# Performance work log

Hardware: AMD Instinct MI355X
Metric: run time of the kernel (lower is better)

The kernel has to match this reference:

```python
import jax, jax.numpy as jnp
import numpy as np

B, I, O = 262144, 128, 128


def setup_inputs() -> dict:
    key = jax.random.key(0)
    k1, k2, k3, k4 = jax.random.split(key, 4)
    # coordinate-like inputs in [-1, 1]
    x = jax.random.uniform(k1, (B, I), dtype=jnp.float32, minval=-1.0, maxval=1.0)
    # complex weight w = s * exp(i*theta): |w| = s (close to 1 so |w|^x stays stable),
    # angle(w) = theta, matching the torch init where complex_weight = cos(a) + i sin(a).
    theta = jax.random.uniform(k2, (O, I), dtype=jnp.float32, minval=-np.pi, maxval=np.pi)
    scale = jnp.exp(0.1 * jax.random.normal(k3, (O, I), dtype=jnp.float32))
    w_real = scale * jnp.cos(theta)
    w_imag = scale * jnp.sin(theta)
    bias = jax.random.uniform(k4, (O,), dtype=jnp.float32, minval=-np.pi, maxval=np.pi)
    return {"x": x, "w_real": w_real, "w_imag": w_imag, "bias": bias}


def reference(x, w_real, w_imag, bias):
    # complex_weight.abs() and .angle() from real/imag components
    abs_w = jnp.sqrt(w_real * w_real + w_imag * w_imag)      # [O, I]
    angle_w = jnp.arctan2(w_imag, w_real)                     # [O, I]
    # magnitude = prod_i |w|_{o,i} ** x_{b,i}  ==  exp(x @ log|w|^T)
    # (algebraic rewrite of the O(B*O*I) pow+prod into a GEMM + pointwise exp)
    magnitude = jnp.exp(jnp.einsum('bi,oi->bo', x, jnp.log(abs_w)))  # [B, O]
    # y = F.linear(x, angle, bias)
    y = jnp.einsum('bi,oi->bo', x, angle_w) + bias            # [B, O]
    return jnp.cos(y) * magnitude
```

## Files before the change

kernel.cpp:

```cpp
#include <hip/hip_runtime.h>


typedef __attribute__((ext_vector_type(8))) short bf16x8;
typedef __attribute__((ext_vector_type(4))) float f32x4;

#define MFMA(a, b, c) __builtin_amdgcn_mfma_f32_16x16x32_bf16((a), (b), (c), 0, 0, 0)

__device__ __forceinline__ unsigned short f2bf_rne(float f) {
    unsigned u = __float_as_uint(f);
    unsigned r = u + 0x7FFFu + ((u >> 16) & 1u);
    return (unsigned short)(r >> 16);
}

__device__ __forceinline__ void bf16_split(float f, unsigned short& hi, unsigned short& lo) {
    unsigned uh = __float_as_uint(f) & 0xFFFF0000u;
    hi = (unsigned short)(uh >> 16);
    lo = f2bf_rne(f - __uint_as_float(uh));
}

__device__ __forceinline__ void cvt_pair(float f0, float f1, unsigned& h, unsigned& l) {
    unsigned u0 = __float_as_uint(f0), u1 = __float_as_uint(f1);
    unsigned uh0 = u0 & 0xFFFF0000u, uh1 = u1 & 0xFFFF0000u;
    h = (uh0 >> 16) | uh1;
    float r0 = f0 - __uint_as_float(uh0);
    float r1 = f1 - __uint_as_float(uh1);
    unsigned v0 = __float_as_uint(r0), v1 = __float_as_uint(r1);
    v0 = v0 + 0x7FFFu + ((v0 >> 16) & 1u);
    v1 = v1 + 0x7FFFu + ((v1 >> 16) & 1u);
    l = (v0 >> 16) | (v1 & 0xFFFF0000u);
}

__global__ void ces_prep(const float* __restrict__ wr, const float* __restrict__ wi,
                         unsigned short* __restrict__ wsplit) {
    int idx = blockIdx.x * 256 + threadIdx.x;
    float a = wr[idx], b = wi[idx];
    float r2 = a * a + b * b;
    float ang = atan2f(b, a);
    float lg = 0.5f * logf(r2);
    unsigned short ah, al, gh, gl;
    bf16_split(ang, ah, al);
    bf16_split(lg, gh, gl);
    wsplit[idx]         = ah;
    wsplit[16384 + idx] = al;
    wsplit[32768 + idx] = gh;
    wsplit[49152 + idx] = gl;
}

#define NT 16

__global__ __launch_bounds__(512, 4) void ces_main(
        const float* __restrict__ x,
        const unsigned short* __restrict__ wsplit,
        const float* __restrict__ bias,
        float* __restrict__ out) {
    __shared__ __align__(16) unsigned short smem[8192];
    char* smemb = (char*)smem;

    const int tid  = threadIdx.x;
    const int wave = tid >> 6;
    const int lane = tid & 63;
    const int quad = lane >> 4;
    const int l16  = lane & 15;
    const int n0   = wave * 16;

    bf16x8 wa_h[4], wa_l[4], wg_h[4], wg_l[4];
    {
        const int o = n0 + l16;
#pragma unroll
        for (int ks = 0; ks < 4; ++ks) {
            const int off = o * 128 + ks * 32 + quad * 8;
            wa_h[ks] = *(const bf16x8*)(wsplit + off);
            wa_l[ks] = *(const bf16x8*)(wsplit + 16384 + off);
            wg_h[ks] = *(const bf16x8*)(wsplit + 32768 + off);
            wg_l[ks] = *(const bf16x8*)(wsplit + 49152 + off);
        }
    }
    const float bias_v = bias[n0 + l16];

    const int wrow = tid >> 5;
    const int wb = (wrow * 256 + (tid & 31) * 8) ^ ((wrow & 7) << 4);
    int rb[4];
#pragma unroll
    for (int ks = 0; ks < 4; ++ks)
        rb[ks] = (l16 * 256 + ks * 64 + quad * 16) ^ ((l16 & 7) << 4);

    const float* xb = x + (size_t)blockIdx.x * (NT * 2048) + tid * 4;

    {
        float4 v = *(const float4*)xb;
        unsigned h0, l0, h1, l1;
        cvt_pair(v.x, v.y, h0, l0);
        cvt_pair(v.z, v.w, h1, l1);
        *(uint2*)(smemb + wb)        = make_uint2(h0, h1);
        *(uint2*)(smemb + wb + 4096) = make_uint2(l0, l1);
    }
    float4 pf = *(const float4*)(xb + 2048);
    __syncthreads();

    for (int i = 0; i < NT; ++i) {
        const int bo = (i & 1) << 13;

        f32x4 accY = {0.f, 0.f, 0.f, 0.f};
        f32x4 accG = {0.f, 0.f, 0.f, 0.f};
#pragma unroll
        for (int ks = 0; ks < 4; ++ks) {
            bf16x8 a_h = *(const bf16x8*)(smemb + (bo + rb[ks]));
            bf16x8 a_l = *(const bf16x8*)(smemb + (bo + rb[ks] + 4096));
            accY = MFMA(a_h, wa_h[ks], accY);
            accG = MFMA(a_h, wg_h[ks], accG);
            accY = MFMA(a_h, wa_l[ks], accY);
            accG = MFMA(a_h, wg_l[ks], accG);
            accY = MFMA(a_l, wa_h[ks], accY);
            accG = MFMA(a_l, wg_h[ks], accG);
        }

        {
            const int nbo = bo ^ 8192;
            unsigned h0, l0, h1, l1;
            cvt_pair(pf.x, pf.y, h0, l0);
            cvt_pair(pf.z, pf.w, h1, l1);
            *(uint2*)(smemb + (nbo + wb))        = make_uint2(h0, h1);
            *(uint2*)(smemb + (nbo + wb + 4096)) = make_uint2(l0, l1);
        }
        {
            int tn = i + 2;
            if (tn > NT - 1) tn = NT - 1;
            pf = *(const float4*)(xb + tn * 2048);
        }
        __syncthreads();

        {
            float* op = out + ((size_t)(blockIdx.x * NT + i) * 16 + quad * 4) * 128 + n0 + l16;
#pragma unroll
            for (int r = 0; r < 4; ++r) {
                float y = accY[r] + bias_v;
                op[(size_t)r * 128] = __cosf(y) * __expf(accG[r]);
            }
        }
    }
}

extern "C" void kernel_launch(void* const* d_in, const int* in_sizes, int n_in,
                              void* d_out, int out_size, void* d_ws, size_t ws_size,
                              hipStream_t stream) {
    const float* x    = (const float*)d_in[0];
    const float* wr   = (const float*)d_in[1];
    const float* wi   = (const float*)d_in[2];
    const float* bias = (const float*)d_in[3];
    float* out = (float*)d_out;
    unsigned short* wsplit = (unsigned short*)d_ws;

    ces_prep<<<64, 256, 0, stream>>>(wr, wi, wsplit);

    ces_main<<<1024, 512, 0, stream>>>(x, wsplit, bias, out);
}
```

Baseline: 252.7 us.

## Halve block to 256 threads with each wave computing two 16-column output tiles

Each block now runs 4 waves instead of 8, and each wave covers 32 output columns using two sets of register-resident weight fragments. Every A fragment read from shared memory is reused across twice as many MFMAs, and each thread stages 8 floats per tile with 16-byte shared stores. The cost is twice the weight registers per wave and fewer waves per block to hide latency, which may lower occupancy. The staging step into the next buffer is also skipped on the final iteration.

```diff
diff --git a/kernel.cpp b/kernel.cpp
--- a/kernel.cpp
+++ b/kernel.cpp
@@ -48,7 +48,7 @@
 
 #define NT 16
 
-__global__ __launch_bounds__(512, 4) void ces_main(
+__global__ __launch_bounds__(256, 2) void ces_main(
         const float* __restrict__ x,
         const unsigned short* __restrict__ wsplit,
         const float* __restrict__ bias,
@@ -61,80 +61,105 @@
     const int lane = tid & 63;
     const int quad = lane >> 4;
     const int l16  = lane & 15;
-    const int n0   = wave * 16;
+    const int n0   = wave * 32;
 
-    bf16x8 wa_h[4], wa_l[4], wg_h[4], wg_l[4];
-    {
-        const int o = n0 + l16;
+    bf16x8 wa_h[2][4], wa_l[2][4], wg_h[2][4], wg_l[2][4];
+#pragma unroll
+    for (int nt = 0; nt < 2; ++nt) {
+        const int o = n0 + nt * 16 + l16;
 #pragma unroll
         for (int ks = 0; ks < 4; ++ks) {
             const int off = o * 128 + ks * 32 + quad * 8;
-            wa_h[ks] = *(const bf16x8*)(wsplit + off);
-            wa_l[ks] = *(const bf16x8*)(wsplit + 16384 + off);
-            wg_h[ks] = *(const bf16x8*)(wsplit + 32768 + off);
-            wg_l[ks] = *(const bf16x8*)(wsplit + 49152 + off);
+            wa_h[nt][ks] = *(const bf16x8*)(wsplit + off);
+            wa_l[nt][ks] = *(const bf16x8*)(wsplit + 16384 + off);
+            wg_h[nt][ks] = *(const bf16x8*)(wsplit + 32768 + off);
+            wg_l[nt][ks] = *(const bf16x8*)(wsplit + 49152 + off);
         }
     }
-    const float bias_v = bias[n0 + l16];
+    float bias_v[2];
+    bias_v[0] = bias[n0 + l16];
+    bias_v[1] = bias[n0 + 16 + l16];
 
-    const int wrow = tid >> 5;
-    const int wb = (wrow * 256 + (tid & 31) * 8) ^ ((wrow & 7) << 4);
+    const int srow = tid >> 4;
+    const int schk = tid & 15;
+    const int wb = (srow * 256 + schk * 16) ^ ((srow & 7) << 4);
+
     int rb[4];
 #pragma unroll
     for (int ks = 0; ks < 4; ++ks)
         rb[ks] = (l16 * 256 + ks * 64 + quad * 16) ^ ((l16 & 7) << 4);
 
-    const float* xb = x + (size_t)blockIdx.x * (NT * 2048) + tid * 4;
+    const float* xb = x + (size_t)blockIdx.x * (NT * 2048) + srow * 128 + schk * 8;
 
     {
-        float4 v = *(const float4*)xb;
-        unsigned h0, l0, h1, l1;
-        cvt_pair(v.x, v.y, h0, l0);
-        cvt_pair(v.z, v.w, h1, l1);
-        *(uint2*)(smemb + wb)        = make_uint2(h0, h1);
-        *(uint2*)(smemb + wb + 4096) = make_uint2(l0, l1);
+        float4 v0 = *(const float4*)(xb);
+        float4 v1 = *(const float4*)(xb + 4);
+        unsigned h0, l0, h1, l1, h2, l2, h3, l3;
+        cvt_pair(v0.x, v0.y, h0, l0);
+        cvt_pair(v0.z, v0.w, h1, l1);
+        cvt_pair(v1.x, v1.y, h2, l2);
+        cvt_pair(v1.z, v1.w, h3, l3);
+        *(uint4*)(smemb + wb)        = make_uint4(h0, h1, h2, h3);
+        *(uint4*)(smemb + wb + 4096) = make_uint4(l0, l1, l2, l3);
     }
-    float4 pf = *(const float4*)(xb + 2048);
+    float4 pf0 = *(const float4*)(xb + 2048);
+    float4 pf1 = *(const float4*)(xb + 2048 + 4);
     __syncthreads();
 
     for (int i = 0; i < NT; ++i) {
         const int bo = (i & 1) << 13;
 
-        f32x4 accY = {0.f, 0.f, 0.f, 0.f};
-        f32x4 accG = {0.f, 0.f, 0.f, 0.f};
+        f32x4 accY[2], accG[2];
+        accY[0] = (f32x4){0.f, 0.f, 0.f, 0.f};
+        accY[1] = (f32x4){0.f, 0.f, 0.f, 0.f};
+        accG[0] = (f32x4){0.f, 0.f, 0.f, 0.f};
+        accG[1] = (f32x4){0.f, 0.f, 0.f, 0.f};
 #pragma unroll
         for (int ks = 0; ks < 4; ++ks) {
             bf16x8 a_h = *(const bf16x8*)(smemb + (bo + rb[ks]));
             bf16x8 a_l = *(const bf16x8*)(smemb + (bo + rb[ks] + 4096));
-            accY = MFMA(a_h, wa_h[ks], accY);
-            accG = MFMA(a_h, wg_h[ks], accG);
-            accY = MFMA(a_h, wa_l[ks], accY);
-            accG = MFMA(a_h, wg_l[ks], accG);
-            accY = MFMA(a_l, wa_h[ks], accY);
-            accG = MFMA(a_l, wg_h[ks], accG);
+            accY[0] = MFMA(a_h, wa_h[0][ks], accY[0]);
+            accG[0] = MFMA(a_h, wg_h[0][ks], accG[0]);
+            accY[1] = MFMA(a_h, wa_h[1][ks], accY[1]);
+            accG[1] = MFMA(a_h, wg_h[1][ks], accG[1]);
+            accY[0] = MFMA(a_h, wa_l[0][ks], accY[0]);
+            accG[0] = MFMA(a_h, wg_l[0][ks], accG[0]);
+            accY[1] = MFMA(a_h, wa_l[1][ks], accY[1]);
+            accG[1] = MFMA(a_h, wg_l[1][ks], accG[1]);
+            accY[0] = MFMA(a_l, wa_h[0][ks], accY[0]);
+            accG[0] = MFMA(a_l, wg_h[0][ks], accG[0]);
+            accY[1] = MFMA(a_l, wa_h[1][ks], accY[1]);
+            accG[1] = MFMA(a_l, wg_h[1][ks], accG[1]);
         }
 
-        {
+        if (i + 1 < NT) {
             const int nbo = bo ^ 8192;
-            unsigned h0, l0, h1, l1;
-            cvt_pair(pf.x, pf.y, h0, l0);
-            cvt_pair(pf.z, pf.w, h1, l1);
-            *(uint2*)(smemb + (nbo + wb))        = make_uint2(h0, h1);
-            *(uint2*)(smemb + (nbo + wb + 4096)) = make_uint2(l0, l1);
+            unsigned h0, l0, h1, l1, h2, l2, h3, l3;
+            cvt_pair(pf0.x, pf0.y, h0, l0);
+            cvt_pair(pf0.z, pf0.w, h1, l1);
+            cvt_pair(pf1.x, pf1.y, h2, l2);
+            cvt_pair(pf1.z, pf1.w, h3, l3);
+            *(uint4*)(smemb + (nbo + wb))        = make_uint4(h0, h1, h2, h3);
+            *(uint4*)(smemb + (nbo + wb + 4096)) = make_uint4(l0, l1, l2, l3);
         }
         {
             int tn = i + 2;
             if (tn > NT - 1) tn = NT - 1;
-            pf = *(const float4*)(xb + tn * 2048);
+            pf0 = *(const float4*)(xb + tn * 2048);
+            pf1 = *(const float4*)(xb + tn * 2048 + 4);
         }
         __syncthreads();
 
         {
-            float* op = out + ((size_t)(blockIdx.x * NT + i) * 16 + quad * 4) * 128 + n0 + l16;
+            const size_t R0 = (size_t)(blockIdx.x * NT + i) * 16;
 #pragma unroll
-            for (int r = 0; r < 4; ++r) {
-                float y = accY[r] + bias_v;
-                op[(size_t)r * 128] = __cosf(y) * __expf(accG[r]);
+            for (int nt = 0; nt < 2; ++nt) {
+                const int o = n0 + nt * 16 + l16;
+#pragma unroll
+                for (int r = 0; r < 4; ++r) {
+                    float y = accY[nt][r] + bias_v[nt];
+                    out[(R0 + quad * 4 + r) * 128 + o] = __cosf(y) * __expf(accG[nt][r]);
+                }
             }
         }
     }
@@ -152,5 +177,5 @@
 
     ces_prep<<<64, 256, 0, stream>>>(wr, wi, wsplit);
 
-    ces_main<<<1024, 512, 0, stream>>>(x, wsplit, bias, out);
+    ces_main<<<1024, 256, 0, stream>>>(x, wsplit, bias, out);
 }
```

After: 254.4 us. About the same (+0.7%).

## Stage 32-row x tiles per barrier and use lightweight LDS-only sync

Applied to the files above, without the earlier changes.

Each pipeline stage now loads and converts 32 rows of x (two 16-row MFMA tiles) instead of 16, so the number of block barriers is halved and each thread issues two float4 loads and 16-byte LDS stores. __syncthreads is replaced by a custom barrier that only waits on LDS counters, and MFMA sections are wrapped in s_setprio. The grid shrinks to 512 blocks, each covering 512 rows, and LDS use doubles to 32 KB per block. This cuts barrier and per-row overhead but lowers the block count and may reduce occupancy.

```diff
diff --git a/kernel.cpp b/kernel.cpp
--- a/kernel.cpp
+++ b/kernel.cpp
@@ -5,6 +5,13 @@
 typedef __attribute__((ext_vector_type(4))) float f32x4;
 
 #define MFMA(a, b, c) __builtin_amdgcn_mfma_f32_16x16x32_bf16((a), (b), (c), 0, 0, 0)
+
+__device__ __forceinline__ void block_sync_lds() {
+    __builtin_amdgcn_sched_barrier(0);
+    asm volatile("s_waitcnt lgkmcnt(0)" ::: "memory");
+    __builtin_amdgcn_s_barrier();
+    __builtin_amdgcn_sched_barrier(0);
+}
 
 __device__ __forceinline__ unsigned short f2bf_rne(float f) {
     unsigned u = __float_as_uint(f);
@@ -46,14 +53,14 @@
     wsplit[49152 + idx] = gl;
 }
 
-#define NT 16
+#define SS 16
 
 __global__ __launch_bounds__(512, 4) void ces_main(
         const float* __restrict__ x,
         const unsigned short* __restrict__ wsplit,
         const float* __restrict__ bias,
         float* __restrict__ out) {
-    __shared__ __align__(16) unsigned short smem[8192];
+    __shared__ __align__(16) unsigned short smem[16384];
     char* smemb = (char*)smem;
 
     const int tid  = threadIdx.x;
@@ -77,66 +84,100 @@
     }
     const float bias_v = bias[n0 + l16];
 
-    const int wrow = tid >> 5;
-    const int wb = (wrow * 256 + (tid & 31) * 8) ^ ((wrow & 7) << 4);
+    const int srow = tid >> 4;
+    const int schk = tid & 15;
+    const int wb = (srow * 256 + schk * 16) ^ ((srow & 7) << 4);
+
     int rb[4];
 #pragma unroll
     for (int ks = 0; ks < 4; ++ks)
         rb[ks] = (l16 * 256 + ks * 64 + quad * 16) ^ ((l16 & 7) << 4);
 
-    const float* xb = x + (size_t)blockIdx.x * (NT * 2048) + tid * 4;
+    const float* xb = x + (size_t)blockIdx.x * 65536 + srow * 128 + schk * 8;
+    float* outb = out + ((size_t)blockIdx.x * 512 + quad * 4) * 128 + n0 + l16;
 
     {
-        float4 v = *(const float4*)xb;
-        unsigned h0, l0, h1, l1;
-        cvt_pair(v.x, v.y, h0, l0);
-        cvt_pair(v.z, v.w, h1, l1);
-        *(uint2*)(smemb + wb)        = make_uint2(h0, h1);
-        *(uint2*)(smemb + wb + 4096) = make_uint2(l0, l1);
+        float4 v0 = *(const float4*)(xb);
+        float4 v1 = *(const float4*)(xb + 4);
+        unsigned h0, l0, h1, l1, h2, l2, h3, l3;
+        cvt_pair(v0.x, v0.y, h0, l0);
+        cvt_pair(v0.z, v0.w, h1, l1);
+        cvt_pair(v1.x, v1.y, h2, l2);
+        cvt_pair(v1.z, v1.w, h3, l3);
+        *(uint4*)(smemb + wb)        = make_uint4(h0, h1, h2, h3);
+        *(uint4*)(smemb + wb + 8192) = make_uint4(l0, l1, l2, l3);
     }
-    float4 pf = *(const float4*)(xb + 2048);
-    __syncthreads();
+    float4 pf0 = *(const float4*)(xb + 4096);
+    float4 pf1 = *(const float4*)(xb + 4096 + 4);
+    block_sync_lds();
 
-    for (int i = 0; i < NT; ++i) {
-        const int bo = (i & 1) << 13;
-
-        f32x4 accY = {0.f, 0.f, 0.f, 0.f};
-        f32x4 accG = {0.f, 0.f, 0.f, 0.f};
-#pragma unroll
-        for (int ks = 0; ks < 4; ++ks) {
-            bf16x8 a_h = *(const bf16x8*)(smemb + (bo + rb[ks]));
-            bf16x8 a_l = *(const bf16x8*)(smemb + (bo + rb[ks] + 4096));
-            accY = MFMA(a_h, wa_h[ks], accY);
-            accG = MFMA(a_h, wg_h[ks], accG);
-            accY = MFMA(a_h, wa_l[ks], accY);
-            accG = MFMA(a_h, wg_l[ks], accG);
-            accY = MFMA(a_l, wa_h[ks], accY);
-            accG = MFMA(a_l, wg_h[ks], accG);
-        }
+    for (int s = 0; s < SS; ++s) {
+        const char* rbase = smemb + (s & 1) * 16384;
+        char* wbase = smemb + ((s & 1) ^ 1) * 16384;
 
         {
-            const int nbo = bo ^ 8192;
-            unsigned h0, l0, h1, l1;
-            cvt_pair(pf.x, pf.y, h0, l0);
-            cvt_pair(pf.z, pf.w, h1, l1);
-            *(uint2*)(smemb + (nbo + wb))        = make_uint2(h0, h1);
-            *(uint2*)(smemb + (nbo + wb + 4096)) = make_uint2(l0, l1);
-        }
-        {
-            int tn = i + 2;
-            if (tn > NT - 1) tn = NT - 1;
-            pf = *(const float4*)(xb + tn * 2048);
-        }
-        __syncthreads();
-
-        {
-            float* op = out + ((size_t)(blockIdx.x * NT + i) * 16 + quad * 4) * 128 + n0 + l16;
+            f32x4 accY = {0.f, 0.f, 0.f, 0.f};
+            f32x4 accG = {0.f, 0.f, 0.f, 0.f};
+            __builtin_amdgcn_s_setprio(1);
+#pragma unroll
+            for (int ks = 0; ks < 4; ++ks) {
+                bf16x8 a_h = *(const bf16x8*)(rbase + rb[ks]);
+                bf16x8 a_l = *(const bf16x8*)(rbase + rb[ks] + 8192);
+                accY = MFMA(a_h, wa_h[ks], accY);
+                accG = MFMA(a_h, wg_h[ks], accG);
+                accY = MFMA(a_h, wa_l[ks], accY);
+                accG = MFMA(a_h, wg_l[ks], accG);
+                accY = MFMA(a_l, wa_h[ks], accY);
+                accG = MFMA(a_l, wg_h[ks], accG);
+            }
+            __builtin_amdgcn_s_setprio(0);
+            float* op = outb + (size_t)(s * 32) * 128;
 #pragma unroll
             for (int r = 0; r < 4; ++r) {
                 float y = accY[r] + bias_v;
                 op[(size_t)r * 128] = __cosf(y) * __expf(accG[r]);
             }
         }
+
+        if (s + 1 < SS) {
+            unsigned h0, l0, h1, l1, h2, l2, h3, l3;
+            cvt_pair(pf0.x, pf0.y, h0, l0);
+            cvt_pair(pf0.z, pf0.w, h1, l1);
+            cvt_pair(pf1.x, pf1.y, h2, l2);
+            cvt_pair(pf1.z, pf1.w, h3, l3);
+            *(uint4*)(wbase + wb)        = make_uint4(h0, h1, h2, h3);
+            *(uint4*)(wbase + wb + 8192) = make_uint4(l0, l1, l2, l3);
+        }
+        if (s + 2 < SS) {
+            pf0 = *(const float4*)(xb + (size_t)(s + 2) * 4096);
+            pf1 = *(const float4*)(xb + (size_t)(s + 2) * 4096 + 4);
+        }
+
+        {
+            f32x4 accY = {0.f, 0.f, 0.f, 0.f};
+            f32x4 accG = {0.f, 0.f, 0.f, 0.f};
+            __builtin_amdgcn_s_setprio(1);
+#pragma unroll
+            for (int ks = 0; ks < 4; ++ks) {
+                bf16x8 a_h = *(const bf16x8*)(rbase + 4096 + rb[ks]);
+                bf16x8 a_l = *(const bf16x8*)(rbase + 4096 + rb[ks] + 8192);
+                accY = MFMA(a_h, wa_h[ks], accY);
+                accG = MFMA(a_h, wg_h[ks], accG);
+                accY = MFMA(a_h, wa_l[ks], accY);
+                accG = MFMA(a_h, wg_l[ks], accG);
+                accY = MFMA(a_l, wa_h[ks], accY);
+                accG = MFMA(a_l, wg_h[ks], accG);
+            }
+            __builtin_amdgcn_s_setprio(0);
+            float* op = outb + (size_t)(s * 32 + 16) * 128;
+#pragma unroll
+            for (int r = 0; r < 4; ++r) {
+                float y = accY[r] + bias_v;
+                op[(size_t)r * 128] = __cosf(y) * __expf(accG[r]);
+            }
+        }
+
+        block_sync_lds();
     }
 }
 
@@ -152,5 +193,5 @@
 
     ces_prep<<<64, 256, 0, stream>>>(wr, wi, wsplit);
 
-    ces_main<<<1024, 512, 0, stream>>>(x, wsplit, bias, out);
+    ces_main<<<512, 512, 0, stream>>>(x, wsplit, bias, out);
 }
```

Measured after the change: 248.0 us. About the same (-1.8%).
